# Performance work log

Hardware: AMD Instinct MI355X
Metric: run time of the kernel (lower is better)

The kernel has to match this reference:

```python
import jax, jax.numpy as jnp
import numpy as np

INPUT_CHANNELS = 3

def setup_inputs() -> dict:
    key = jax.random.key(0)
    kx, ky = jax.random.split(key)
    x = jax.random.normal(kx, (8, 4096, 3), dtype=jnp.float32)
    y = jax.random.normal(ky, (8, 4096, 3), dtype=jnp.float32)
    return {"x": x, "y": y}

def reference(x, y):
    # Match torch: truncate both clouds to common num_points and input_channels.
    num_points = min(x.shape[1], y.shape[1])
    x = x[:, :num_points, :INPUT_CHANNELS]
    y = y[:, :num_points, :INPUT_CHANNELS]
    # pdist[b, i, j] = ||x_i||^2 + ||y_j||^2 - 2 x_i . y_j  (squared Euclidean)
    x2 = jnp.sum(x * x, axis=-1)          # [B, N]
    y2 = jnp.sum(y * y, axis=-1)          # [B, N]
    zz = jnp.einsum('bic,bjc->bij', x, y) # [B, N, N]
    pdist = x2[:, :, None] + y2[:, None, :] - 2.0 * zz
    # min over i (dim 1): nearest x for each y; min over j (dim 2): nearest y for each x
    loss = jnp.mean(jnp.min(pdist, axis=1)) + jnp.mean(jnp.min(pdist, axis=2))
    return loss * 0.005
```

## Files before the change

kernel.cpp:

```cpp
#include <hip/hip_runtime.h>

#define NPTS 4096
#define NB   8
#define TOT  (2 * NB * NPTS)

typedef __attribute__((ext_vector_type(8)))  short          bf16x8;
typedef __attribute__((ext_vector_type(8)))  unsigned short u16x8;
typedef __attribute__((ext_vector_type(16))) float          f32x16;

__device__ __forceinline__ unsigned short bf16_rne(float f) {
    unsigned u = __float_as_uint(f);
    u += 0x7FFFu + ((u >> 16) & 1u);
    return (unsigned short)(u >> 16);
}
__device__ __forceinline__ float bf16_f(unsigned short s) {
    return __uint_as_float(((unsigned)s) << 16);
}


__global__ __launch_bounds__(256) void prep_b(
    const float* __restrict__ x, const float* __restrict__ y,
    unsigned short* __restrict__ Bform, unsigned* __restrict__ smax,
    float* __restrict__ out)
{
    int i   = blockIdx.x * 256 + threadIdx.x;
    int cid = i >> 12;
    int p   = i & 4095;
    const float* src = (cid < 8) ? x + ((size_t)cid * NPTS + p) * 3
                                 : y + ((size_t)(cid - 8) * NPTS + p) * 3;
    float c0 = src[0], c1 = src[1], c2 = src[2];
    float h  = -0.5f * (c0 * c0 + c1 * c1 + c2 * c2);

    unsigned short h0 = bf16_rne(c0), h1 = bf16_rne(c1), h2 = bf16_rne(c2);
    unsigned short l0 = bf16_rne(c0 - bf16_f(h0));
    unsigned short l1 = bf16_rne(c1 - bf16_f(h1));
    unsigned short l2 = bf16_rne(c2 - bf16_f(h2));
    unsigned short hh = bf16_rne(h);
    unsigned short hl = bf16_rne(h - bf16_f(hh));

    u16x8 blo, bhi;
    blo[0]=h0; blo[1]=h1; blo[2]=h2; blo[3]=h0; blo[4]=h1; blo[5]=h2; blo[6]=l0; blo[7]=l1;
    bhi[0]=l2; bhi[1]=hh; bhi[2]=hl; bhi[3]=0; bhi[4]=0; bhi[5]=0; bhi[6]=0; bhi[7]=0;

    int u = p >> 5, pos = p & 31;
    size_t base = ((size_t)cid << 17) + (size_t)u * 1024 + (size_t)pos * 16;
    *(u16x8*)((char*)Bform + base)       = blo;
    *(u16x8*)((char*)Bform + base + 512) = bhi;

    smax[i] = 0u;
    if (i == 0) *out = 0.f;
}

__global__ __launch_bounds__(256, 2) void chamfer_mfma(
    const float* __restrict__ x, const float* __restrict__ y,
    const unsigned short* __restrict__ Bform,
    unsigned* __restrict__ smax)
{
    __shared__ float buf[4][64][33];

    const int bid  = blockIdx.x;
    const int dirb = bid >> 5;
    const int sub  = bid & 31;
    const int iblk = sub >> 2;
    const int jq   = sub & 3;

    const int tid = threadIdx.x;
    const int w   = tid >> 6;
    const int l   = tid & 63;
    const int g   = l >> 5;
    const int pos = l & 31;

    const float* Araw = (dirb < 8) ? x + (size_t)dirb * NPTS * 3
                                   : y + (size_t)(dirb - 8) * NPTS * 3;
    const char* Bbase = (const char*)Bform + ((size_t)(dirb ^ 8) << 17);

    const int it0 = iblk * 16 + w * 4;
    bf16x8 afr[4];
    #pragma unroll
    for (int t = 0; t < 4; ++t) {
        const float* ap = Araw + (size_t)((it0 + t) * 32 + pos) * 3;
        float c0 = ap[0], c1 = ap[1], c2 = ap[2];
        unsigned short h0 = bf16_rne(c0), h1 = bf16_rne(c1), h2 = bf16_rne(c2);
        unsigned short l0 = bf16_rne(c0 - bf16_f(h0));
        unsigned short l1 = bf16_rne(c1 - bf16_f(h1));
        unsigned short l2 = bf16_rne(c2 - bf16_f(h2));
        const short ONE = (short)0x3F80;
        bf16x8 alo, ahi;
        alo[0]=(short)h0; alo[1]=(short)h1; alo[2]=(short)h2; alo[3]=(short)l0;
        alo[4]=(short)l1; alo[5]=(short)l2; alo[6]=(short)h0; alo[7]=(short)h1;
        ahi[0]=(short)h2; ahi[1]=ONE; ahi[2]=ONE; ahi[3]=0;
        ahi[4]=0; ahi[5]=0; ahi[6]=0; ahi[7]=0;
        #pragma unroll
        for (int e = 0; e < 8; ++e) afr[t][e] = g ? ahi[e] : alo[e];
    }

    f32x16 zc;
    #pragma unroll
    for (int r = 0; r < 16; ++r) zc[r] = 0.f;

    f32x16 run[4];
    #pragma unroll
    for (int t = 0; t < 4; ++t)
        #pragma unroll
        for (int r = 0; r < 16; ++r) run[t][r] = -3.0e38f;

    f32x16 p0, p1;
    #pragma unroll
    for (int r = 0; r < 16; ++r) { p0[r] = -3.0e38f; p1[r] = -3.0e38f; }

    const char* Bq = Bbase + (size_t)(jq * 32) * 1024
                           + (size_t)g * 512 + (size_t)pos * 16;

    bf16x8 cb0 = *(const bf16x8*)(Bq);
    bf16x8 cb1 = *(const bf16x8*)(Bq + 1024);
    bf16x8 cb2 = *(const bf16x8*)(Bq + 2048);
    bf16x8 cb3 = *(const bf16x8*)(Bq + 3072);

#define STAGE(T, B0, B1, RP)                                                    \
    {                                                                           \
        f32x16 d0 = __builtin_amdgcn_mfma_f32_32x32x16_bf16(afr[T], B0, zc, 0, 0, 0); \
        f32x16 d1 = __builtin_amdgcn_mfma_f32_32x32x16_bf16(afr[T], B1, zc, 0, 0, 0); \
        _Pragma("unroll")                                                       \
        for (int r = 0; r < 16; ++r)                                            \
            run[RP][r] = fmaxf(fmaxf(p0[r], p1[r]), run[RP][r]);                \
        p0 = d0; p1 = d1;                                                       \
    }

    #pragma unroll 1
    for (int j = 0; j < 32; j += 4) {
        bf16x8 nb0, nb1, nb2, nb3;
        if (j < 28) {
            const char* Bn = Bq + (size_t)(j + 4) * 1024;
            nb0 = *(const bf16x8*)(Bn);
            nb1 = *(const bf16x8*)(Bn + 1024);
            nb2 = *(const bf16x8*)(Bn + 2048);
            nb3 = *(const bf16x8*)(Bn + 3072);
        }
        STAGE(0, cb0, cb1, 3)
        STAGE(1, cb0, cb1, 0)
        STAGE(2, cb0, cb1, 1)
        STAGE(3, cb0, cb1, 2)
        STAGE(0, cb2, cb3, 3)
        STAGE(1, cb2, cb3, 0)
        STAGE(2, cb2, cb3, 1)
        STAGE(3, cb2, cb3, 2)
        if (j < 28) { cb0 = nb0; cb1 = nb1; cb2 = nb2; cb3 = nb3; }
    }
#undef STAGE

    #pragma unroll
    for (int r = 0; r < 16; ++r)
        run[3][r] = fmaxf(fmaxf(p0[r], p1[r]), run[3][r]);

    #pragma unroll
    for (int ph = 0; ph < 2; ++ph) {
        if (ph) __syncthreads();
        #pragma unroll
        for (int tl = 0; tl < 2; ++tl) {
            const int t = 2 * ph + tl;
            #pragma unroll
            for (int r = 0; r < 16; ++r) {
                int rowin = (r & 3) + 8 * (r >> 2) + 4 * g;
                buf[w][tl * 32 + rowin][pos] = run[t][r];
            }
        }
        __syncthreads();

        float m = buf[w][l][0];
        #pragma unroll
        for (int k = 1; k < 32; ++k) m = fmaxf(m, buf[w][l][k]);
        int idx = dirb * 4096 + iblk * 512 + w * 128 + 2 * ph * 32 + l;
        unsigned bits = __float_as_uint(m);
        unsigned mu = (bits & 0x80000000u) ? ~bits : (bits | 0x80000000u);
        atomicMax(&smax[idx], mu);
    }
}

__global__ __launch_bounds__(256) void reduce_kernel(
    const unsigned* __restrict__ smax,
    const float* __restrict__ x, const float* __restrict__ y,
    float* __restrict__ out)
{
    const int stride = 64 * 256;
    int tid = blockIdx.x * 256 + threadIdx.x;
    float s = 0.f;
    for (int k = tid; k < TOT; k += stride) {
        unsigned u = smax[k];
        unsigned bits = (u & 0x80000000u) ? (u & 0x7FFFFFFFu) : ~u;
        int cid = k >> 12, p = k & 4095;
        const float* ap = (cid < 8) ? x + ((size_t)cid * NPTS + p) * 3
                                    : y + ((size_t)(cid - 8) * NPTS + p) * 3;
        float a0 = ap[0], a1 = ap[1], a2 = ap[2];
        s += __uint_as_float(bits) - 0.5f * (a0 * a0 + a1 * a1 + a2 * a2);
    }

    #pragma unroll
    for (int off = 32; off > 0; off >>= 1)
        s += __shfl_down(s, off);

    __shared__ float redb[4];
    const int lane = threadIdx.x & 63, wave = threadIdx.x >> 6;
    if (lane == 0) redb[wave] = s;
    __syncthreads();
    if (threadIdx.x == 0) {
        float t = redb[0] + redb[1] + redb[2] + redb[3];
        atomicAdd(out, t * (-2.0f * 0.005f / 32768.f));
    }
}

extern "C" void kernel_launch(void* const* d_in, const int* in_sizes, int n_in,
                              void* d_out, int out_size, void* d_ws, size_t ws_size,
                              hipStream_t stream) {
    const float* x = (const float*)d_in[0];
    const float* y = (const float*)d_in[1];
    float* out = (float*)d_out;

    unsigned short* Bform = (unsigned short*)d_ws;
    unsigned*       smax  = (unsigned*)((char*)d_ws + (2u << 20));

    prep_b<<<dim3(TOT / 256), dim3(256), 0, stream>>>(x, y, Bform, smax, out);
    chamfer_mfma<<<dim3(512), dim3(256), 0, stream>>>(x, y, Bform, smax);
    reduce_kernel<<<dim3(64), dim3(256), 0, stream>>>(smax, x, y, out);
}
```

Before: 69.74 us.

## Fuse B-operand prep into main kernel via LDS and drop atomics

Removes the separate prep kernel: each block now converts its 1024-point B slice into bf16 hi/lo split form directly in shared memory, then runs the MFMA loop reading B from LDS instead of global. The per-row atomicMax into a global buffer is replaced by plain stores of per-(block, jq) partial maxima, which the reduce kernel combines over four slots. This removes one launch, the global Bform round-trip and the atomics. In exchange each block spends time converting B up front and uses 32KB more LDS, which could reduce occupancy.

```diff
diff --git a/kernel.cpp b/kernel.cpp
--- a/kernel.cpp
+++ b/kernel.cpp
@@ -18,44 +18,11 @@
 }
 
 
-__global__ __launch_bounds__(256) void prep_b(
-    const float* __restrict__ x, const float* __restrict__ y,
-    unsigned short* __restrict__ Bform, unsigned* __restrict__ smax,
-    float* __restrict__ out)
-{
-    int i   = blockIdx.x * 256 + threadIdx.x;
-    int cid = i >> 12;
-    int p   = i & 4095;
-    const float* src = (cid < 8) ? x + ((size_t)cid * NPTS + p) * 3
-                                 : y + ((size_t)(cid - 8) * NPTS + p) * 3;
-    float c0 = src[0], c1 = src[1], c2 = src[2];
-    float h  = -0.5f * (c0 * c0 + c1 * c1 + c2 * c2);
-
-    unsigned short h0 = bf16_rne(c0), h1 = bf16_rne(c1), h2 = bf16_rne(c2);
-    unsigned short l0 = bf16_rne(c0 - bf16_f(h0));
-    unsigned short l1 = bf16_rne(c1 - bf16_f(h1));
-    unsigned short l2 = bf16_rne(c2 - bf16_f(h2));
-    unsigned short hh = bf16_rne(h);
-    unsigned short hl = bf16_rne(h - bf16_f(hh));
-
-    u16x8 blo, bhi;
-    blo[0]=h0; blo[1]=h1; blo[2]=h2; blo[3]=h0; blo[4]=h1; blo[5]=h2; blo[6]=l0; blo[7]=l1;
-    bhi[0]=l2; bhi[1]=hh; bhi[2]=hl; bhi[3]=0; bhi[4]=0; bhi[5]=0; bhi[6]=0; bhi[7]=0;
-
-    int u = p >> 5, pos = p & 31;
-    size_t base = ((size_t)cid << 17) + (size_t)u * 1024 + (size_t)pos * 16;
-    *(u16x8*)((char*)Bform + base)       = blo;
-    *(u16x8*)((char*)Bform + base + 512) = bhi;
-
-    smax[i] = 0u;
-    if (i == 0) *out = 0.f;
-}
-
 __global__ __launch_bounds__(256, 2) void chamfer_mfma(
     const float* __restrict__ x, const float* __restrict__ y,
-    const unsigned short* __restrict__ Bform,
-    unsigned* __restrict__ smax)
+    float* __restrict__ smaxp, float* __restrict__ out)
 {
+    __shared__ unsigned short sB[16384];
     __shared__ float buf[4][64][33];
 
     const int bid  = blockIdx.x;
@@ -70,9 +37,34 @@
     const int g   = l >> 5;
     const int pos = l & 31;
 
+    if (bid == 0 && tid == 0) *out = 0.f;
+
     const float* Araw = (dirb < 8) ? x + (size_t)dirb * NPTS * 3
                                    : y + (size_t)(dirb - 8) * NPTS * 3;
-    const char* Bbase = (const char*)Bform + ((size_t)(dirb ^ 8) << 17);
+    const int bcid = dirb ^ 8;
+    const float* Braw = (bcid < 8) ? x + (size_t)bcid * NPTS * 3
+                                   : y + (size_t)(bcid - 8) * NPTS * 3;
+
+    #pragma unroll
+    for (int k = 0; k < 4; ++k) {
+        int p = tid + k * 256;
+        const float* src = Braw + (size_t)(jq * 1024 + p) * 3;
+        float c0 = src[0], c1 = src[1], c2 = src[2];
+        float h  = -0.5f * (c0 * c0 + c1 * c1 + c2 * c2);
+        unsigned short h0 = bf16_rne(c0), h1 = bf16_rne(c1), h2 = bf16_rne(c2);
+        unsigned short l0 = bf16_rne(c0 - bf16_f(h0));
+        unsigned short l1 = bf16_rne(c1 - bf16_f(h1));
+        unsigned short l2 = bf16_rne(c2 - bf16_f(h2));
+        unsigned short hh = bf16_rne(h);
+        unsigned short hl = bf16_rne(h - bf16_f(hh));
+        u16x8 blo, bhi;
+        blo[0]=h0; blo[1]=h1; blo[2]=h2; blo[3]=h0; blo[4]=h1; blo[5]=h2; blo[6]=l0; blo[7]=l1;
+        bhi[0]=l2; bhi[1]=hh; bhi[2]=hl; bhi[3]=0; bhi[4]=0; bhi[5]=0; bhi[6]=0; bhi[7]=0;
+        int u = p >> 5, ppos = p & 31;
+        char* dst = (char*)sB + (size_t)u * 1024 + (size_t)ppos * 16;
+        *(u16x8*)dst         = blo;
+        *(u16x8*)(dst + 512) = bhi;
+    }
 
     const int it0 = iblk * 16 + w * 4;
     bf16x8 afr[4];
@@ -94,6 +86,8 @@
         for (int e = 0; e < 8; ++e) afr[t][e] = g ? ahi[e] : alo[e];
     }
 
+    __syncthreads();
+
     f32x16 zc;
     #pragma unroll
     for (int r = 0; r < 16; ++r) zc[r] = 0.f;
@@ -108,8 +102,7 @@
     #pragma unroll
     for (int r = 0; r < 16; ++r) { p0[r] = -3.0e38f; p1[r] = -3.0e38f; }
 
-    const char* Bq = Bbase + (size_t)(jq * 32) * 1024
-                           + (size_t)g * 512 + (size_t)pos * 16;
+    const char* Bq = (const char*)sB + (size_t)g * 512 + (size_t)pos * 16;
 
     bf16x8 cb0 = *(const bf16x8*)(Bq);
     bf16x8 cb1 = *(const bf16x8*)(Bq + 1024);
@@ -152,6 +145,7 @@
     for (int r = 0; r < 16; ++r)
         run[3][r] = fmaxf(fmaxf(p0[r], p1[r]), run[3][r]);
 
+    const int slotbase = (((dirb * 8 + iblk) * 4 + jq) << 9);
     #pragma unroll
     for (int ph = 0; ph < 2; ++ph) {
         if (ph) __syncthreads();
@@ -169,15 +163,12 @@
         float m = buf[w][l][0];
         #pragma unroll
         for (int k = 1; k < 32; ++k) m = fmaxf(m, buf[w][l][k]);
-        int idx = dirb * 4096 + iblk * 512 + w * 128 + 2 * ph * 32 + l;
-        unsigned bits = __float_as_uint(m);
-        unsigned mu = (bits & 0x80000000u) ? ~bits : (bits | 0x80000000u);
-        atomicMax(&smax[idx], mu);
+        smaxp[slotbase + w * 128 + ph * 64 + l] = m;
     }
 }
 
 __global__ __launch_bounds__(256) void reduce_kernel(
-    const unsigned* __restrict__ smax,
+    const float* __restrict__ smaxp,
     const float* __restrict__ x, const float* __restrict__ y,
     float* __restrict__ out)
 {
@@ -185,13 +176,15 @@
     int tid = blockIdx.x * 256 + threadIdx.x;
     float s = 0.f;
     for (int k = tid; k < TOT; k += stride) {
-        unsigned u = smax[k];
-        unsigned bits = (u & 0x80000000u) ? (u & 0x7FFFFFFFu) : ~u;
-        int cid = k >> 12, p = k & 4095;
-        const float* ap = (cid < 8) ? x + ((size_t)cid * NPTS + p) * 3
-                                    : y + ((size_t)(cid - 8) * NPTS + p) * 3;
+        int cid = k >> 12, ri = k & 4095;
+        int iblk = ri >> 9, rem = ri & 511;
+        const float* base = smaxp + (((cid * 8 + iblk) * 4) << 9) + rem;
+        float m = fmaxf(fmaxf(base[0], base[512]),
+                        fmaxf(base[1024], base[1536]));
+        const float* ap = (cid < 8) ? x + ((size_t)cid * NPTS + ri) * 3
+                                    : y + ((size_t)(cid - 8) * NPTS + ri) * 3;
         float a0 = ap[0], a1 = ap[1], a2 = ap[2];
-        s += __uint_as_float(bits) - 0.5f * (a0 * a0 + a1 * a1 + a2 * a2);
+        s += m - 0.5f * (a0 * a0 + a1 * a1 + a2 * a2);
     }
 
     #pragma unroll
@@ -215,10 +208,8 @@
     const float* y = (const float*)d_in[1];
     float* out = (float*)d_out;
 
-    unsigned short* Bform = (unsigned short*)d_ws;
-    unsigned*       smax  = (unsigned*)((char*)d_ws + (2u << 20));
-
-    prep_b<<<dim3(TOT / 256), dim3(256), 0, stream>>>(x, y, Bform, smax, out);
-    chamfer_mfma<<<dim3(512), dim3(256), 0, stream>>>(x, y, Bform, smax);
-    reduce_kernel<<<dim3(64), dim3(256), 0, stream>>>(smax, x, y, out);
-}
+    float* smaxp = (float*)d_ws;
+
+    chamfer_mfma<<<dim3(512), dim3(256), 0, stream>>>(x, y, smaxp, out);
+    reduce_kernel<<<dim3(64), dim3(256), 0, stream>>>(smaxp, x, y, out);
+}
```

New measurement: 66.49 us, median of 3. 4.7% less time.
